# Kernel tuning notes

Measured on AMD Instinct MI355X. Metric: run time of the kernel, lower is better.

Reference implementation:

```python
import jax, jax.numpy as jnp
import numpy as np
from jax import lax

B, CIN, H, W = 64, 3, 64, 64
HID = 128          # hidden_dim == embedding_dim
K = 1024           # num_embeddings
BETA = 0.25        # commitment cost


def _conv(x, w, b, stride):
    # torch Conv2d, padding=0, NCHW / OIHW weights
    y = lax.conv_general_dilated(x, w, (stride, stride), 'VALID',
                                 dimension_numbers=('NCHW', 'OIHW', 'NCHW'))
    return y + b[None, :, None, None]


def _conv_transpose(x, w, b, stride):
    # torch ConvTranspose2d, padding=0; w is [Cin, Cout, kh, kw] (torch layout)
    kh, kw = w.shape[2], w.shape[3]
    w2 = jnp.flip(w, (2, 3)).transpose(1, 0, 2, 3)  # -> OIHW, spatially flipped
    y = lax.conv_general_dilated(x, w2, (1, 1),
                                 [(kh - 1, kh - 1), (kw - 1, kw - 1)],
                                 lhs_dilation=(stride, stride),
                                 dimension_numbers=('NCHW', 'OIHW', 'NCHW'))
    return y + b[None, :, None, None]


def setup_inputs() -> dict:
    key = jax.random.key(0)
    ks = jax.random.split(key, 10)
    s = 0.05
    return {
        'x':      jax.random.normal(ks[0], (B, CIN, H, W), jnp.float32),
        'enc_w1': jax.random.normal(ks[1], (HID, CIN, 4, 4), jnp.float32) * s,
        'enc_b1': jnp.zeros((HID,), jnp.float32),
        'enc_w2': jax.random.normal(ks[2], (HID, HID, 2, 2), jnp.float32) * s,
        'enc_b2': jnp.zeros((HID,), jnp.float32),
        'codebook': jax.random.uniform(ks[3], (K, HID), jnp.float32,
                                       minval=-1.0 / K, maxval=1.0 / K),
        'dec_w1': jax.random.normal(ks[4], (HID, HID, 2, 2), jnp.float32) * s,
        'dec_b1': jnp.zeros((HID,), jnp.float32),
        'dec_w2': jax.random.normal(ks[5], (HID, CIN, 4, 4), jnp.float32) * s,
        'dec_b2': jnp.zeros((CIN,), jnp.float32),
    }


def reference(x, enc_w1, enc_b1, enc_w2, enc_b2, codebook,
              dec_w1, dec_b1, dec_w2, dec_b2):
    # ---- encoder ----
    z = jax.nn.relu(_conv(x, enc_w1, enc_b1, 2))
    z = jax.nn.relu(_conv(z, enc_w2, enc_b2, 1))   # [B, HID, 30, 30]

    # ---- vector quantizer (faithful to torch reshape semantics) ----
    D = HID
    flat = z.reshape(-1, D)                        # [N, D], C-order rows
    # squared euclidean distances (argmin identical to torch.cdist argmin)
    d2 = (jnp.sum(flat * flat, axis=1, keepdims=True)
          - 2.0 * flat @ codebook.T
          + jnp.sum(codebook * codebook, axis=1)[None, :])  # [N, K]
    idx = jnp.argmin(d2, axis=1)                   # [N]
    quantized = codebook[idx].reshape(z.shape)

    e_latent = jnp.mean((lax.stop_gradient(quantized) - z) ** 2)
    q_latent = jnp.mean((quantized - lax.stop_gradient(z)) ** 2)
    loss = q_latent + BETA * e_latent

    q_st = z + lax.stop_gradient(quantized - z)    # straight-through

    n = flat.shape[0]
    avg_probs = jnp.zeros((K,), z.dtype).at[idx].add(1.0) / n
    perplexity = jnp.exp(-jnp.sum(avg_probs * jnp.log(avg_probs + 1e-10)))

    # ---- decoder ----
    y = jax.nn.relu(_conv_transpose(q_st, dec_w1, dec_b1, 1))
    x_recon = _conv_transpose(y, dec_w2, dec_b2, 2)  # [B, 3, 64, 64]
    return x_recon, loss, perplexity
```

## Files before the change

kernel.cpp:

```cpp
#include <hip/hip_runtime.h>

#define B_    64
#define CIN_  3
#define HW_   64
#define HID_  128
#define K_    1024
#define H1_   31
#define H2_   30
#define NROWS_ 57600
#define NELEM_ 7372800

typedef __bf16 bf16_t;
typedef __attribute__((ext_vector_type(8))) __bf16 bf16x8;
typedef __attribute__((ext_vector_type(4))) float f32x4;

__global__ __launch_bounds__(256) void wprep_k(const float* __restrict__ ew1,
    const float* __restrict__ ew2, const float* __restrict__ dw1,
    const float* __restrict__ dw2, const float* __restrict__ cb,
    bf16_t* __restrict__ wc1, bf16_t* __restrict__ wc2,
    bf16_t* __restrict__ wd1, bf16_t* __restrict__ wt2,
    bf16_t* __restrict__ cbb, float* __restrict__ cnorm,
    unsigned* __restrict__ hist, float* __restrict__ sse) {
  int id = blockIdx.x * 256 + threadIdx.x;
  int t = id >> 14, co = (id >> 7) & 127, ci = id & 127;
  wc2[id] = (bf16_t)ew2[(co * 128 + ci) * 4 + t];
  wd1[id] = (bf16_t)dw1[(ci * 128 + co) * 4 + (3 - t)];
  if (id < 8192) {
    int n = id >> 9, k = id & 511;
    int tap = k >> 7, c = k & 127;
    if (n < 12) {
      int nco = n >> 2, ph = (n >> 1) & 1, pw = n & 1;
      int off = (tap >> 1) * 8 + (tap & 1) * 2;
      wt2[id] = (bf16_t)dw2[c * 48 + nco * 16 + ph * 4 + pw + off];
    } else {
      wt2[id] = (bf16_t)0.f;
    }
    int c1 = id >> 6, k1 = id & 63;
    wc1[id] = (bf16_t)(k1 < 48 ? ew1[c1 * 48 + k1] : 0.f);
  }
  if (id < K_) {
    float s0 = 0.f;
    for (int d = 0; d < HID_; d += 4) {
      float4 v = *(const float4*)&cb[id * HID_ + d];
      bf16_t tt[4] = {(bf16_t)v.x, (bf16_t)v.y, (bf16_t)v.z, (bf16_t)v.w};
      *(ushort4*)&((ushort*)cbb)[id * HID_ + d] = *(ushort4*)tt;
      float f0 = (float)tt[0], f1 = (float)tt[1];
      float f2 = (float)tt[2], f3 = (float)tt[3];
      s0 += f0 * f0 + f1 * f1 + f2 * f2 + f3 * f3;
    }
    cnorm[id] = s0;
    hist[id] = 0u;
  }
  if (id == 0) *sse = 0.f;
}

__global__ __launch_bounds__(256, 2) void conv1m_k(const float* __restrict__ x,
    const bf16_t* __restrict__ wc1, const float* __restrict__ bias,
    ushort* __restrict__ z1t) {
  __shared__ __align__(16) bf16_t as_[64 * 72];
  __shared__ __align__(16) bf16_t bs_[128 * 72];
  int b = blockIdx.x >> 4, rt = blockIdx.x & 15;
  int tid = threadIdx.x, wv = tid >> 6, ln = tid & 63;
  const float* xb = x + (size_t)b * 12288;
  #pragma unroll
  for (int it = 0; it < 16; ++it) {
    int e = it * 256 + tid;
    int p = e >> 6, k = e & 63;
    float v = 0.f;
    if (k < 48) {
      int ci = k >> 4, kh = (k >> 2) & 3, kw = k & 3;
      int row = 2 * rt + (p >> 5); if (row > 30) row = 30;
      int col = p & 31;            if (col > 30) col = 30;
      v = xb[ci * 4096 + (2 * row + kh) * 64 + 2 * col + kw];
    }
    as_[p * 72 + k] = (bf16_t)v;
  }
  {
    const float4* wg = (const float4*)wc1;
    #pragma unroll
    for (int it = 0; it < 4; ++it) {
      int fi = it * 256 + tid;
      int co = fi >> 3, k8 = fi & 7;
      *(float4*)&bs_[co * 72 + k8 * 8] = wg[fi];
    }
  }
  __syncthreads();
  int q = ln >> 4, l = ln & 15;
  f32x4 acc8[8];
  #pragma unroll
  for (int c = 0; c < 8; ++c) acc8[c] = (f32x4){0.f, 0.f, 0.f, 0.f};
  bf16x8 af[2];
  #pragma unroll
  for (int kk = 0; kk < 2; ++kk)
    af[kk] = *(const bf16x8*)&as_[(wv * 16 + l) * 72 + kk * 32 + q * 8];
  #pragma unroll
  for (int cot = 0; cot < 8; ++cot) {
    #pragma unroll
    for (int kk = 0; kk < 2; ++kk) {
      bf16x8 bf = *(const bf16x8*)&bs_[(cot * 16 + l) * 72 + kk * 32 + q * 8];
      acc8[cot] = __builtin_amdgcn_mfma_f32_16x16x32_bf16(af[kk], bf,
                                                          acc8[cot], 0, 0, 0);
    }
  }
  #pragma unroll
  for (int cot = 0; cot < 8; ++cot) {
    int co = cot * 16 + l;
    float bv = bias[co];
    #pragma unroll
    for (int r = 0; r < 4; ++r) {
      int pos = wv * 16 + q * 4 + r;
      int prow = 2 * rt + (pos >> 5), pcol = pos & 31;
      if (prow < 31 && pcol < 31) {
        float v = fmaxf(acc8[cot][r] + bv, 0.f);
        bf16_t h = (bf16_t)v;
        z1t[((size_t)(b * 1024 + prow * 32 + pcol)) * 128 + co] = *(ushort*)&h;
      }
    }
  }
}

__global__ __launch_bounds__(256, 2) void conv2m_k(const bf16_t* __restrict__ z1t,
    const bf16_t* __restrict__ wc2, const float* __restrict__ bias,
    ushort* __restrict__ zbuf) {
  __shared__ __align__(16) bf16_t as_[98 * 136];
  __shared__ __align__(16) bf16_t bs_[128 * 136];
  int blk = blockIdx.x;
  int b = blk / 15, rt = blk % 15;
  int tid = threadIdx.x, wv = tid >> 6, ln = tid & 63;
  const float4* src = (const float4*)(z1t + ((size_t)b * 1024 + rt * 64) * 128);
  #pragma unroll
  for (int s = 0; s < 7; ++s) {
    int f = s * 256 + tid;
    if (f < 1568) {
      int lp = f >> 4, c16 = f & 15;
      *(float4*)&as_[lp * 136 + c16 * 8] = src[f];
    }
  }
  int m = wv * 16 + (ln & 15), q = ln >> 4;
  f32x4 acc8[8];
  #pragma unroll
  for (int c = 0; c < 8; ++c) acc8[c] = (f32x4){0.f, 0.f, 0.f, 0.f};
  const float4* w4 = (const float4*)wc2;
  #pragma unroll
  for (int t = 0; t < 4; ++t) {
    __syncthreads();
    #pragma unroll
    for (int s = 0; s < 8; ++s) {
      int f = s * 256 + tid;
      int co = f >> 4, c16 = f & 15;
      *(float4*)&bs_[co * 136 + c16 * 8] = w4[t * 2048 + f];
    }
    __syncthreads();
    int off = (t >> 1) * 32 + (t & 1);
    bf16x8 af[4];
    #pragma unroll
    for (int kk = 0; kk < 4; ++kk)
      af[kk] = *(const bf16x8*)&as_[(m + off) * 136 + kk * 32 + q * 8];
    #pragma unroll
    for (int cot = 0; cot < 8; ++cot) {
      #pragma unroll
      for (int kk = 0; kk < 4; ++kk) {
        bf16x8 bf = *(const bf16x8*)&bs_[(cot * 16 + (ln & 15)) * 136 +
                                         kk * 32 + q * 8];
        acc8[cot] = __builtin_amdgcn_mfma_f32_16x16x32_bf16(af[kk], bf,
                                                            acc8[cot], 0, 0, 0);
      }
    }
  }
  #pragma unroll
  for (int cot = 0; cot < 8; ++cot) {
    int co = cot * 16 + (ln & 15);
    float bv = bias[co];
    #pragma unroll
    for (int r = 0; r < 4; ++r) {
      int mo = wv * 16 + q * 4 + r;
      int ocol = mo & 31;
      if (ocol < 30) {
        int orow = rt * 2 + (mo >> 5);
        float v = fmaxf(acc8[cot][r] + bv, 0.f);
        bf16_t h = (bf16_t)v;
        zbuf[(size_t)(b * HID_ + co) * 900 + orow * 30 + ocol] = *(ushort*)&h;
      }
    }
  }
}

__global__ __launch_bounds__(256, 2) void vq1_k(const bf16_t* __restrict__ zb,
    const bf16_t* __restrict__ cbb, const float* __restrict__ cnorm,
    int* __restrict__ idxArr, unsigned* __restrict__ hist,
    float* __restrict__ sse) {
  __shared__ __align__(16) bf16_t zs[64 * 136];
  __shared__ __align__(16) bf16_t cbs[128 * 136];
  __shared__ unsigned long long red[64 * 16];
  __shared__ float cns[K_];
  int n0 = blockIdx.x * 64;
  int tid = threadIdx.x;
  int wv = tid >> 6, ln = tid & 63;
  {
    const float4* zg4 = (const float4*)(zb + (size_t)n0 * HID_);
    #pragma unroll
    for (int s = 0; s < 4; ++s) {
      int f = s * 256 + tid;
      int row = f >> 4, seg = f & 15;
      *(float4*)&zs[row * 136 + seg * 8] = zg4[f];
    }
    ((float4*)cns)[tid] = ((const float4*)cnorm)[tid];
  }
  __syncthreads();
  bf16x8 afr[4];
  #pragma unroll
  for (int kk = 0; kk < 4; ++kk)
    afr[kk] = *(const bf16x8*)&zs[(wv * 16 + (ln & 15)) * 136 + kk * 32 +
                                  (ln >> 4) * 8];
  unsigned long long best[4] = {~0ull, ~0ull, ~0ull, ~0ull};
  const float4* cg4 = (const float4*)cbb;
  for (int c0 = 0; c0 < K_; c0 += 128) {
    __syncthreads();
    #pragma unroll
    for (int s = 0; s < 8; ++s) {
      int f = s * 256 + tid;
      int code = f >> 4, seg = f & 15;
      *(float4*)&cbs[code * 136 + seg * 8] = cg4[(c0 + code) * 16 + seg];
    }
    __syncthreads();
    #pragma unroll 2
    for (int t = 0; t < 8; ++t) {
      f32x4 acc = {0.f, 0.f, 0.f, 0.f};
      #pragma unroll
      for (int kk = 0; kk < 4; ++kk) {
        bf16x8 bfr = *(const bf16x8*)&cbs[(t * 16 + (ln & 15)) * 136 +
                                          kk * 32 + (ln >> 4) * 8];
        acc = __builtin_amdgcn_mfma_f32_16x16x32_bf16(afr[kk], bfr, acc,
                                                      0, 0, 0);
      }
      int code = c0 + t * 16 + (ln & 15);
      float cn = cns[code];
      #pragma unroll
      for (int r = 0; r < 4; ++r) {
        float dist = cn - 2.f * acc[r];
        unsigned u = __float_as_uint(dist);
        u = (u & 0x80000000u) ? ~u : (u | 0x80000000u);
        unsigned long long p = ((unsigned long long)u << 32) | (unsigned)code;
        if (p < best[r]) best[r] = p;
      }
    }
  }
  __syncthreads();
  #pragma unroll
  for (int r = 0; r < 4; ++r)
    red[(wv * 16 + (ln >> 4) * 4 + r) * 16 + (ln & 15)] = best[r];
  __syncthreads();
  if (tid < 64) {
    unsigned long long b = ~0ull;
    #pragma unroll
    for (int c = 0; c < 16; ++c) {
      unsigned long long p = red[tid * 16 + c];
      if (p < b) b = p;
    }
    int bi = (int)(b & 0xffffffffu);
    idxArr[n0 + tid] = bi;
    atomicAdd(&hist[bi], 1u);
    unsigned hi = (unsigned)(b >> 32);
    unsigned orig = (hi & 0x80000000u) ? (hi & 0x7fffffffu) : ~hi;
    float dmin = __uint_as_float(orig);
    float zn = 0.f;
    #pragma unroll
    for (int s = 0; s < 16; ++s) {
      bf16x8 v = *(const bf16x8*)&zs[tid * 136 + s * 8];
      #pragma unroll
      for (int e = 0; e < 8; ++e) {
        float fv = (float)v[e];
        zn = fmaf(fv, fv, zn);
      }
    }
    float se = zn + dmin;
    #pragma unroll
    for (int o = 32; o > 0; o >>= 1) se += __shfl_down(se, o, 64);
    if (tid == 0) atomicAdd(sse, se);
  }
}

__global__ __launch_bounds__(256) void tqz_k(const bf16_t* __restrict__ cbb,
    const int* __restrict__ idxArr, ushort* __restrict__ qt) {
  __shared__ ushort t[60 * 128];
  int bid = blockIdx.x, tid = threadIdx.x;
  if (bid < 960) {
    int b = bid / 15, st = bid % 15;
    int s0 = st * 60;
    #pragma unroll
    for (int it = 0; it < 8; ++it) {
      int task = it * 256 + tid;
      if (task < 1920) {
        int sc = task >> 7, c = task & 127;
        int f = b * 115200 + c * 900 + s0 + sc * 4;
        int n = f >> 7, d = f & 127;
        int k = idxArr[n];
        ushort4 v = *(const ushort4*)((const ushort*)cbb + k * 128 + d);
        t[(sc * 4 + 0) * 128 + c] = v.x;
        t[(sc * 4 + 1) * 128 + c] = v.y;
        t[(sc * 4 + 2) * 128 + c] = v.z;
        t[(sc * 4 + 3) * 128 + c] = v.w;
      }
    }
    __syncthreads();
    #pragma unroll
    for (int it = 0; it < 4; ++it) {
      int task = it * 256 + tid;
      if (task < 960) {
        int sl = task >> 4, c16 = task & 15;
        int s = s0 + sl;
        int h = s / 30, w = s - h * 30;
        int p = (h + 1) * 32 + (w + 1);
        *(uint4*)&qt[((size_t)(b * 1024 + p)) * 128 + c16 * 8] =
            *(uint4*)&t[sl * 128 + c16 * 8];
      }
    }
  } else {
    int zb_ = (bid - 960) * 4;
    uint4 zz = {0u, 0u, 0u, 0u};
    for (int e = tid; e < 4 * 124 * 16; e += 256) {
      int bb = zb_ + e / (124 * 16);
      int rem = e % (124 * 16);
      int pe = rem >> 4, s16 = rem & 15;
      int p;
      if (pe < 32) p = pe;
      else if (pe < 64) p = 31 * 32 + (pe - 32);
      else {
        int idx = pe - 64;
        p = (1 + (idx >> 1)) * 32 + ((idx & 1) ? 31 : 0);
      }
      *(uint4*)&qt[((size_t)(bb * 1024 + p)) * 128 + s16 * 8] = zz;
    }
  }
}

__global__ __launch_bounds__(256, 2) void convt1m_k(const bf16_t* __restrict__ qt,
    const bf16_t* __restrict__ wd1, const float* __restrict__ bias,
    ushort* __restrict__ yt) {
  __shared__ __align__(16) bf16_t as_[98 * 136];
  __shared__ __align__(16) bf16_t bs_[128 * 136];
  int blk = blockIdx.x;
  int b = blk >> 4, rt = blk & 15;
  int tid = threadIdx.x, wv = tid >> 6, ln = tid & 63;
  {
    uint4 zz = {0u, 0u, 0u, 0u};
    ushort* ytb = yt + (size_t)b * 1156 * 128;
    int nrows = (rt < 15) ? 2 : 1;
    int r0 = 2 * rt + 1;
    for (int e = tid; e < nrows * 48; e += 256) {
      int rr = e / 48, rem = e % 48, cc = rem / 16, s16 = rem % 16;
      int col = (cc == 0) ? 0 : (cc == 1 ? 32 : 33);
      *(uint4*)&ytb[((size_t)((r0 + rr) * 34 + col)) * 128 + s16 * 8] = zz;
    }
    if (rt == 0)
      for (int e = tid; e < 34 * 16; e += 256)
        *(uint4*)&ytb[((size_t)(e >> 4)) * 128 + (e & 15) * 8] = zz;
    if (rt == 15)
      for (int e = tid; e < 2 * 34 * 16; e += 256) {
        int rr = 32 + e / 544, rem = e % 544;
        *(uint4*)&ytb[((size_t)(rr * 34 + (rem >> 4))) * 128 + (rem & 15) * 8]
            = zz;
      }
  }
  const float4* src = (const float4*)(qt + (size_t)b * 1024 * 128);
  #pragma unroll
  for (int s = 0; s < 7; ++s) {
    int f = s * 256 + tid;
    if (f < 1568) {
      int lp = f >> 4, c16 = f & 15;
      int gr = rt * 64 + lp;
      if (gr > 1023) gr = 1023;
      *(float4*)&as_[lp * 136 + c16 * 8] = src[gr * 16 + c16];
    }
  }
  int m = wv * 16 + (ln & 15), q = ln >> 4;
  f32x4 acc8[8];
  #pragma unroll
  for (int c = 0; c < 8; ++c) acc8[c] = (f32x4){0.f, 0.f, 0.f, 0.f};
  const float4* w4 = (const float4*)wd1;
  #pragma unroll
  for (int t = 0; t < 4; ++t) {
    __syncthreads();
    #pragma unroll
    for (int s = 0; s < 8; ++s) {
      int f = s * 256 + tid;
      int co = f >> 4, c16 = f & 15;
      *(float4*)&bs_[co * 136 + c16 * 8] = w4[t * 2048 + f];
    }
    __syncthreads();
    int off = (t >> 1) * 32 + (t & 1);
    bf16x8 af[4];
    #pragma unroll
    for (int kk = 0; kk < 4; ++kk)
      af[kk] = *(const bf16x8*)&as_[(m + off) * 136 + kk * 32 + q * 8];
    #pragma unroll
    for (int cot = 0; cot < 8; ++cot) {
      #pragma unroll
      for (int kk = 0; kk < 4; ++kk) {
        bf16x8 bf = *(const bf16x8*)&bs_[(cot * 16 + (ln & 15)) * 136 +
                                         kk * 32 + q * 8];
        acc8[cot] = __builtin_amdgcn_mfma_f32_16x16x32_bf16(af[kk], bf,
                                                            acc8[cot], 0, 0, 0);
      }
    }
  }
  #pragma unroll
  for (int cot = 0; cot < 8; ++cot) {
    int co = cot * 16 + (ln & 15);
    float bv = bias[co];
    #pragma unroll
    for (int r = 0; r < 4; ++r) {
      int mo = wv * 16 + q * 4 + r;
      int orow = rt * 2 + (mo >> 5), ocol = mo & 31;
      if (orow < 31 && ocol < 31) {
        float v = fmaxf(acc8[cot][r] + bv, 0.f);
        bf16_t h = (bf16_t)v;
        yt[((size_t)b * 1156 + (orow + 1) * 34 + (ocol + 1)) * 128 + co] =
            *(ushort*)&h;
      }
    }
  }
}

__global__ __launch_bounds__(256, 2) void convt2m_k(const bf16_t* __restrict__ yt,
    const bf16_t* __restrict__ wt2, const float* __restrict__ bias,
    const unsigned* __restrict__ hist, const float* __restrict__ sse,
    float* __restrict__ out) {
  __shared__ __align__(16) bf16_t as_[128 * 136];
  __shared__ float redf[256];
  int b = blockIdx.x >> 4, rt = blockIdx.x & 15;
  int tid = threadIdx.x, wv = tid >> 6, ln = tid & 63;
  const float4* src = (const float4*)(yt + ((size_t)b * 1156 + rt * 68) * 128);
  #pragma unroll
  for (int s = 0; s < 8; ++s) {
    int f = s * 256 + tid;
    int lp = f >> 4, c16 = f & 15;
    *(float4*)&as_[lp * 136 + c16 * 8] = src[f];
  }
  __syncthreads();
  int mloc = wv * 16 + (ln & 15), q = ln >> 4;
  int qh = mloc >> 5, qw = mloc & 31;
  int base = (qh + 1) * 34 + qw + 1;
  f32x4 acc = {0.f, 0.f, 0.f, 0.f};
  #pragma unroll
  for (int kc = 0; kc < 16; ++kc) {
    int tap = kc >> 2;
    int toff = (tap & 1) + (tap >> 1) * 34;
    bf16x8 af = *(const bf16x8*)&as_[(base - toff) * 136 +
                                     (kc & 3) * 32 + q * 8];
    bf16x8 bf = *(const bf16x8*)&wt2[(size_t)(ln & 15) * 512 + kc * 32 + q * 8];
    acc = __builtin_amdgcn_mfma_f32_16x16x32_bf16(af, bf, acc, 0, 0, 0);
  }
  __syncthreads();
  float* bb = (float*)as_;
  #pragma unroll
  for (int r = 0; r < 4; ++r)
    bb[(wv * 16 + q * 4 + r) * 16 + (ln & 15)] = acc[r];
  __syncthreads();
  if (tid < 192) {
    int row_id = tid >> 4;
    int co = row_id >> 2, ohoff = row_id & 3;
    int qhl = ohoff >> 1, ph = ohoff & 1;
    float bv = bias[co];
    int ow0 = (tid & 15) * 4;
    float tmp[4];
    #pragma unroll
    for (int e = 0; e < 4; ++e) {
      int ow = ow0 + e;
      tmp[e] = bb[(qhl * 32 + (ow >> 1)) * 16 + co * 4 + ph * 2 + (ow & 1)]
               + bv;
    }
    *(float4*)&out[((size_t)(b * 3 + co)) * 4096 + (rt * 4 + ohoff) * 64 + ow0]
        = *(float4*)tmp;
  }
  if (blockIdx.x == 0) {
    float e = 0.f;
    for (int k = tid; k < K_; k += 256) {
      float p = (float)hist[k] * (1.0f / (float)NROWS_);
      e += p * logf(p + 1e-10f);
    }
    redf[tid] = e;
    __syncthreads();
    #pragma unroll
    for (int t = 128; t > 0; t >>= 1) {
      if (tid < t) redf[tid] += redf[tid + t];
      __syncthreads();
    }
    if (tid == 0) {
      out[786432] = 1.25f * (*sse) * (1.0f / (float)NELEM_);
      out[786433] = expf(-redf[0]);
    }
  }
}

extern "C" void kernel_launch(void* const* d_in, const int* in_sizes, int n_in,
                              void* d_out, int out_size, void* d_ws,
                              size_t ws_size, hipStream_t stream) {
  (void)in_sizes; (void)n_in; (void)out_size; (void)ws_size;
  const float* x   = (const float*)d_in[0];
  const float* ew1 = (const float*)d_in[1];
  const float* eb1 = (const float*)d_in[2];
  const float* ew2 = (const float*)d_in[3];
  const float* eb2 = (const float*)d_in[4];
  const float* cb  = (const float*)d_in[5];
  const float* dw1 = (const float*)d_in[6];
  const float* db1 = (const float*)d_in[7];
  const float* dw2 = (const float*)d_in[8];
  const float* db2 = (const float*)d_in[9];
  float* out = (float*)d_out;
  char* ws = (char*)d_ws;

  ushort*   yt    = (ushort*)(ws);
  bf16_t*   z1t   = (bf16_t*)(ws + 65175552);
  bf16_t*   qt    = (bf16_t*)(ws + 65175552);
  ushort*   zbuf  = (ushort*)(ws + 81985536);
  bf16_t*   cbb   = (bf16_t*)(ws + 96731136);
  bf16_t*   wc2   = (bf16_t*)(ws + 96993280);
  bf16_t*   wd1   = (bf16_t*)(ws + 97124352);
  int*      idxArr= (int*)(ws + 97255424);
  unsigned* hist  = (unsigned*)(ws + 97485824);
  float*    cnorm = (float*)(ws + 97489920);
  float*    sse   = (float*)(ws + 97494016);
  bf16_t*   wt2   = (bf16_t*)(ws + 97497088);
  bf16_t*   wc1   = (bf16_t*)(ws + 97513472);

  wprep_k<<<dim3(256), dim3(256), 0, stream>>>(ew1, ew2, dw1, dw2, cb,
                                               wc1, wc2, wd1, wt2,
                                               cbb, cnorm, hist, sse);
  conv1m_k<<<dim3(1024), dim3(256), 0, stream>>>(x, wc1, eb1, (ushort*)z1t);
  conv2m_k<<<dim3(960), dim3(256), 0, stream>>>(z1t, wc2, eb2, zbuf);
  vq1_k<<<dim3(900), dim3(256), 0, stream>>>((const bf16_t*)zbuf, cbb, cnorm,
                                             idxArr, hist, sse);
  tqz_k<<<dim3(976), dim3(256), 0, stream>>>(cbb, idxArr, (ushort*)qt);
  convt1m_k<<<dim3(1024), dim3(256), 0, stream>>>(qt, wd1, db1, yt);
  convt2m_k<<<dim3(1024), dim3(256), 0, stream>>>((const bf16_t*)yt, wt2, db2,
                                                  hist, sse, out);
}
```

Baseline: 231.2 us.

## Switch VQ distance kernel to 32x32 MFMA tiles with shuffle-based argmin reduction

The VQ distance kernel now uses 32x32x16 bf16 MFMA tiles instead of 16x16x32. Each wave handles a 32-row by 64-code block per codebook chunk rather than 16 rows by 128 codes. The per-lane argmin candidates are reduced across lanes with xor shuffles before a small shared-memory cross-wave merge, which replaces the larger 64x16 shared reduction table. This is meant to cut LDS fragment reads per FLOP and shrink reduction traffic, at the cost of more registers (16 accumulators and 16 64-bit bests per lane) and more shuffle work.

```diff
diff --git a/kernel.cpp b/kernel.cpp
--- a/kernel.cpp
+++ b/kernel.cpp
@@ -13,6 +13,7 @@
 typedef __bf16 bf16_t;
 typedef __attribute__((ext_vector_type(8))) __bf16 bf16x8;
 typedef __attribute__((ext_vector_type(4))) float f32x4;
+typedef __attribute__((ext_vector_type(16))) float f32x16;
 
 __global__ __launch_bounds__(256) void wprep_k(const float* __restrict__ ew1,
     const float* __restrict__ ew2, const float* __restrict__ dw1,
@@ -191,8 +192,8 @@
     float* __restrict__ sse) {
   __shared__ __align__(16) bf16_t zs[64 * 136];
   __shared__ __align__(16) bf16_t cbs[128 * 136];
-  __shared__ unsigned long long red[64 * 16];
   __shared__ float cns[K_];
+  __shared__ unsigned long long red2[128];
   int n0 = blockIdx.x * 64;
   int tid = threadIdx.x;
   int wv = tid >> 6, ln = tid & 63;
@@ -207,12 +208,15 @@
     ((float4*)cns)[tid] = ((const float4*)cnorm)[tid];
   }
   __syncthreads();
-  bf16x8 afr[4];
-  #pragma unroll
-  for (int kk = 0; kk < 4; ++kk)
-    afr[kk] = *(const bf16x8*)&zs[(wv * 16 + (ln & 15)) * 136 + kk * 32 +
-                                  (ln >> 4) * 8];
-  unsigned long long best[4] = {~0ull, ~0ull, ~0ull, ~0ull};
+  int mt = wv & 1, npair = wv >> 1;
+  int lr = ln & 31, lh = ln >> 5;
+  bf16x8 afr[8];
+  #pragma unroll
+  for (int ks = 0; ks < 8; ++ks)
+    afr[ks] = *(const bf16x8*)&zs[(mt * 32 + lr) * 136 + ks * 16 + lh * 8];
+  unsigned long long best[16];
+  #pragma unroll
+  for (int r = 0; r < 16; ++r) best[r] = ~0ull;
   const float4* cg4 = (const float4*)cbb;
   for (int c0 = 0; c0 < K_; c0 += 128) {
     __syncthreads();
@@ -223,40 +227,54 @@
       *(float4*)&cbs[code * 136 + seg * 8] = cg4[(c0 + code) * 16 + seg];
     }
     __syncthreads();
-    #pragma unroll 2
-    for (int t = 0; t < 8; ++t) {
-      f32x4 acc = {0.f, 0.f, 0.f, 0.f};
+    #pragma unroll
+    for (int nt2 = 0; nt2 < 2; ++nt2) {
+      int nt = npair * 2 + nt2;
+      f32x16 acc = {0.f, 0.f, 0.f, 0.f, 0.f, 0.f, 0.f, 0.f,
+                    0.f, 0.f, 0.f, 0.f, 0.f, 0.f, 0.f, 0.f};
       #pragma unroll
-      for (int kk = 0; kk < 4; ++kk) {
-        bf16x8 bfr = *(const bf16x8*)&cbs[(t * 16 + (ln & 15)) * 136 +
-                                          kk * 32 + (ln >> 4) * 8];
-        acc = __builtin_amdgcn_mfma_f32_16x16x32_bf16(afr[kk], bfr, acc,
+      for (int ks = 0; ks < 8; ++ks) {
+        bf16x8 bfr = *(const bf16x8*)&cbs[(nt * 32 + lr) * 136 +
+                                          ks * 16 + lh * 8];
+        acc = __builtin_amdgcn_mfma_f32_32x32x16_bf16(afr[ks], bfr, acc,
                                                       0, 0, 0);
       }
-      int code = c0 + t * 16 + (ln & 15);
+      int code = c0 + nt * 32 + lr;
       float cn = cns[code];
+      unsigned long long lc = (unsigned)code;
       #pragma unroll
-      for (int r = 0; r < 4; ++r) {
+      for (int r = 0; r < 16; ++r) {
         float dist = cn - 2.f * acc[r];
         unsigned u = __float_as_uint(dist);
         u = (u & 0x80000000u) ? ~u : (u | 0x80000000u);
-        unsigned long long p = ((unsigned long long)u << 32) | (unsigned)code;
+        unsigned long long p = ((unsigned long long)u << 32) | lc;
         if (p < best[r]) best[r] = p;
       }
     }
   }
-  __syncthreads();
-  #pragma unroll
-  for (int r = 0; r < 4; ++r)
-    red[(wv * 16 + (ln >> 4) * 4 + r) * 16 + (ln & 15)] = best[r];
+  #pragma unroll
+  for (int r = 0; r < 16; ++r) {
+    unsigned long long b = best[r];
+    #pragma unroll
+    for (int o = 16; o > 0; o >>= 1) {
+      unsigned long long ob = __shfl_xor(b, o, 64);
+      if (ob < b) b = ob;
+    }
+    best[r] = b;
+  }
+  if (lr == 0) {
+    #pragma unroll
+    for (int r = 0; r < 16; ++r)
+      red2[((mt * 2 + npair) * 2 + lh) * 16 + r] = best[r];
+  }
   __syncthreads();
   if (tid < 64) {
-    unsigned long long b = ~0ull;
-    #pragma unroll
-    for (int c = 0; c < 16; ++c) {
-      unsigned long long p = red[tid * 16 + c];
-      if (p < b) b = p;
-    }
+    int fmt = tid >> 5, r32 = tid & 31;
+    int half = (r32 >> 2) & 1;
+    int reg = (r32 & 3) | (((r32 >> 3) & 3) << 2);
+    unsigned long long b0 = red2[((fmt * 2 + 0) * 2 + half) * 16 + reg];
+    unsigned long long b1 = red2[((fmt * 2 + 1) * 2 + half) * 16 + reg];
+    unsigned long long b = (b1 < b0) ? b1 : b0;
     int bi = (int)(b & 0xffffffffu);
     idxArr[n0 + tid] = bi;
     atomicAdd(&hist[bi], 1u);
```

Result: no change. 227.0 us (-1.8%).
